# Optimization experiments

Hardware: AMD Instinct MI355X
Metric: run time of the kernel (lower is better)

Reference implementation:

```python
import jax, jax.numpy as jnp
import numpy as np

N_NODES = 100000
N_EDGES = 3200000
NEG_SLOPE = 0.2


def setup_inputs() -> dict:
    key = jax.random.key(0)
    k = jax.random.split(key, 7)
    feat = jax.random.normal(k[0], (N_NODES, 256), dtype=jnp.float32)
    W_fc = jax.random.normal(k[1], (64, 256), dtype=jnp.float32) * 0.05
    attn_l = jax.random.normal(k[2], (4, 16), dtype=jnp.float32) * 0.1
    attn_r = jax.random.normal(k[3], (4, 16), dtype=jnp.float32) * 0.1
    W_res = jax.random.normal(k[4], (64, 256), dtype=jnp.float32) * 0.05
    src = jax.random.randint(k[5], (N_EDGES,), 0, N_NODES, dtype=jnp.int32)
    dst = jax.random.randint(k[6], (N_EDGES,), 0, N_NODES, dtype=jnp.int32)
    return {"feat": feat, "W_fc": W_fc, "attn_l": attn_l, "attn_r": attn_r,
            "W_res": W_res, "src": src, "dst": dst}


def reference(feat, W_fc, attn_l, attn_r, W_res, src, dst):
    N = feat.shape[0]
    H, D = attn_l.shape
    # Linear projection -> per-head features [N, H, D]
    feat_src = (feat @ W_fc.T).reshape(N, H, D)
    # Per-node attention logits [N, H]
    el = jnp.einsum('nhd,hd->nh', feat_src, attn_l)
    er = jnp.einsum('nhd,hd->nh', feat_src, attn_r)
    # fused_gat: per-edge leaky-relu score, edge softmax over dst, scatter-sum
    e = jax.nn.leaky_relu(el[src] + er[dst], negative_slope=NEG_SLOPE)  # [E, H]
    emax = jax.ops.segment_max(e, dst, num_segments=N)  # [N, H]
    emax = jnp.where(jnp.isfinite(emax), emax, 0.0)  # zero-degree safety
    ee = jnp.exp(e - emax[dst])  # [E, H]
    denom = jax.ops.segment_sum(ee, dst, num_segments=N)  # [N, H]
    alpha = ee / jnp.maximum(denom[dst], 1e-20)  # [E, H]
    # weighted aggregation of source features -> [N, H, D]
    rst = jax.ops.segment_sum(alpha[:, :, None] * feat_src[src], dst,
                              num_segments=N)
    # residual connection (res_fc always present in this module)
    resval = (feat @ W_res.T).reshape(N, H, D)
    return rst + resval
```

## Files before the change

### kernel.cpp

```cpp
#include <hip/hip_runtime.h>
#include <hip/hip_bf16.h>


#define F_IN 256
#define O_OUT 64
#define NEG_SLOPE 0.2f
#define CHUNK 4096
#define RMAX 2048

using frag_ab = __attribute__((ext_vector_type(8))) short;
using frag_cd = __attribute__((ext_vector_type(4))) float;

__device__ __forceinline__ float lrelu(float x) {
    return x >= 0.0f ? x : NEG_SLOPE * x;
}

__device__ __forceinline__ unsigned short f2bf(float f) {
    unsigned int u = __float_as_uint(f);
    unsigned int r = (u + 0x7fffu + ((u >> 16) & 1u)) >> 16;
    return (unsigned short)r;
}
__device__ __forceinline__ float bflo(unsigned int p) {
    return __uint_as_float(p << 16);
}
__device__ __forceinline__ float bfhi(unsigned int p) {
    return __uint_as_float(p & 0xffff0000u);
}

__global__ __launch_bounds__(256) void wprep_kernel(
    const float* __restrict__ Wfc, const float* __restrict__ Wres,
    unsigned short* __restrict__ Bf)
{
    int tid = blockIdx.x * 256 + threadIdx.x;
    int ct = tid >> 9;
    int lane = tid & 63;
    int ks = (tid >> 6) & 7;
    int col = ct * 16 + (lane & 15);
    int kbase = ks * 32 + (lane >> 4) * 8;
    const float* srcW = (col < 64) ? (Wfc + (size_t)col * 256 + kbase)
                                   : (Wres + (size_t)(col - 64) * 256 + kbase);
    unsigned short* dstp = Bf + (size_t)tid * 8;
#pragma unroll
    for (int i = 0; i < 8; ++i) dstp[i] = f2bf(srcW[i]);
}

__global__ __launch_bounds__(256) void proj_mfma_kernel(
    const float* __restrict__ feat, const unsigned short* __restrict__ Bf,
    const float* __restrict__ attn_l, const float* __restrict__ attn_r,
    unsigned short* __restrict__ fsb, float* __restrict__ el,
    float* __restrict__ er, float* __restrict__ out,
    float* __restrict__ denom_zero, int N)
{
    __shared__ __align__(16) unsigned short sA[64 * 280];
    const int t = threadIdx.x;
    const int lane = t & 63;
    const int w = t >> 6;
    const int n0 = blockIdx.x * 64;
    if (n0 >= N) return;

    frag_ab bfrag[2][8];
    {
        const unsigned short* bp = Bf + (size_t)lane * 8;
#pragma unroll
        for (int j = 0; j < 2; ++j)
#pragma unroll
            for (int ks = 0; ks < 8; ++ks)
                bfrag[j][ks] = *(const frag_ab*)(bp + (size_t)((2 * w + j) * 8 + ks) * 512);
    }

    if (denom_zero && n0 * 4 + t < N * 4) denom_zero[n0 * 4 + t] = 0.0f;

    for (int i = 0; i < 8; ++i) {
        int f = i * 256 + t;
        int row = f >> 5, c8 = f & 31;
        int n = n0 + row;
        float4 v0 = make_float4(0.f, 0.f, 0.f, 0.f), v1 = v0;
        if (n < N) {
            const float4* p = (const float4*)(feat + (size_t)n * F_IN + c8 * 8);
            v0 = p[0]; v1 = p[1];
        }
        frag_ab pack;
        pack[0] = (short)f2bf(v0.x); pack[1] = (short)f2bf(v0.y);
        pack[2] = (short)f2bf(v0.z); pack[3] = (short)f2bf(v0.w);
        pack[4] = (short)f2bf(v1.x); pack[5] = (short)f2bf(v1.y);
        pack[6] = (short)f2bf(v1.z); pack[7] = (short)f2bf(v1.w);
        *(frag_ab*)(&sA[row * 280 + c8 * 8]) = pack;
    }
    __syncthreads();

    frag_cd acc[4][2];
#pragma unroll
    for (int rt = 0; rt < 4; ++rt)
#pragma unroll
        for (int j = 0; j < 2; ++j)
            acc[rt][j] = (frag_cd){0.f, 0.f, 0.f, 0.f};

#pragma unroll
    for (int ks = 0; ks < 8; ++ks) {
        frag_ab af[4];
#pragma unroll
        for (int rt = 0; rt < 4; ++rt) {
            int row = rt * 16 + (lane & 15);
            int c8 = ks * 4 + (lane >> 4);
            af[rt] = *(const frag_ab*)(&sA[row * 280 + c8 * 8]);
        }
#pragma unroll
        for (int rt = 0; rt < 4; ++rt)
#pragma unroll
            for (int j = 0; j < 2; ++j)
                acc[rt][j] = __builtin_amdgcn_mfma_f32_16x16x32_bf16(
                    af[rt], bfrag[j][ks], acc[rt][j], 0, 0, 0);
    }

    const int colq = lane & 15;
    const int quad = lane >> 4;
    if (w < 2) {
#pragma unroll
        for (int j = 0; j < 2; ++j) {
            int h = 2 * w + j;
            float al = attn_l[h * 16 + colq];
            float ar = attn_r[h * 16 + colq];
#pragma unroll
            for (int rt = 0; rt < 4; ++rt)
#pragma unroll
                for (int r = 0; r < 4; ++r) {
                    int node = n0 + rt * 16 + quad * 4 + r;
                    float v = acc[rt][j][r];
                    if (node < N) fsb[(size_t)node * O_OUT + h * 16 + colq] = f2bf(v);
                    float pl = v * al, pr = v * ar;
                    pl += __shfl_xor(pl, 1); pr += __shfl_xor(pr, 1);
                    pl += __shfl_xor(pl, 2); pr += __shfl_xor(pr, 2);
                    pl += __shfl_xor(pl, 4); pr += __shfl_xor(pr, 4);
                    pl += __shfl_xor(pl, 8); pr += __shfl_xor(pr, 8);
                    if (colq == 0 && node < N) {
                        el[(size_t)node * 4 + h] = pl;
                        er[(size_t)node * 4 + h] = pr;
                    }
                }
        }
    } else {
#pragma unroll
        for (int j = 0; j < 2; ++j) {
            int cb = 32 * (w - 2) + 16 * j;
#pragma unroll
            for (int rt = 0; rt < 4; ++rt)
#pragma unroll
                for (int r = 0; r < 4; ++r) {
                    int node = n0 + rt * 16 + quad * 4 + r;
                    if (node < N)
                        out[(size_t)node * O_OUT + cb + colq] = acc[rt][j][r];
                }
        }
    }
}

__global__ __launch_bounds__(256) void bucket_count_kernel(
    const int* __restrict__ dst, int* __restrict__ histT, int E, int B, int R)
{
    __shared__ int h[RMAX];
    int b = blockIdx.x, t = threadIdx.x;
    for (int i = t; i < R; i += 256) h[i] = 0;
    __syncthreads();
    int base = b * CHUNK;
    for (int i = t; i < CHUNK; i += 256) {
        int e = base + i;
        if (e < E) atomicAdd(&h[dst[e] >> 7], 1);
    }
    __syncthreads();
    for (int i = t; i < R; i += 256) histT[(size_t)i * B + b] = h[i];
}

__global__ __launch_bounds__(256) void scan_block_kernel(
    const int* __restrict__ counts, int* __restrict__ outp,
    int* __restrict__ bsums, int n)
{
    int t = threadIdx.x;
    int base = blockIdx.x * 1024 + t * 4;
    int c0 = 0, c1 = 0, c2 = 0, c3 = 0;
    if (base + 3 < n) {
        int4 v = *(const int4*)(counts + base);
        c0 = v.x; c1 = v.y; c2 = v.z; c3 = v.w;
    } else {
        if (base     < n) c0 = counts[base];
        if (base + 1 < n) c1 = counts[base + 1];
        if (base + 2 < n) c2 = counts[base + 2];
        if (base + 3 < n) c3 = counts[base + 3];
    }
    int tsum = c0 + c1 + c2 + c3;
    int inc = tsum;
    int lane = t & 63, wid = t >> 6;
#pragma unroll
    for (int o = 1; o < 64; o <<= 1) {
        int v = __shfl_up(inc, o);
        if (lane >= o) inc += v;
    }
    __shared__ int wsum[4];
    if (lane == 63) wsum[wid] = inc;
    __syncthreads();
    int woff = 0;
#pragma unroll
    for (int w = 0; w < 4; ++w)
        if (w < wid) woff += wsum[w];
    int excl = woff + inc - tsum;
    int e0 = excl, e1 = excl + c0, e2 = e1 + c1, e3 = e2 + c2;
    if (base + 3 < n) {
        *(int4*)(outp + base) = make_int4(e0, e1, e2, e3);
    } else {
        if (base     < n) outp[base]     = e0;
        if (base + 1 < n) outp[base + 1] = e1;
        if (base + 2 < n) outp[base + 2] = e2;
        if (base + 3 < n) outp[base + 3] = e3;
    }
    if (t == 255) bsums[blockIdx.x] = wsum[0] + wsum[1] + wsum[2] + wsum[3];
}

__global__ void scan_bsums_kernel(int* __restrict__ bsums, int nb)
{
    int lane = threadIdx.x;
    int carry = 0;
    for (int c = 0; c * 64 < nb; ++c) {
        int i = c * 64 + lane;
        int v = (i < nb) ? bsums[i] : 0;
        int inc = v;
#pragma unroll
        for (int o = 1; o < 64; o <<= 1) {
            int u = __shfl_up(inc, o);
            if (lane >= o) inc += u;
        }
        if (i < nb) bsums[i] = carry + inc - v;
        carry += __shfl(inc, 63);
    }
}

__global__ __launch_bounds__(256) void scan_final_kernel(
    int* __restrict__ outp, const int* __restrict__ bsums, int n, int total)
{
    int i = blockIdx.x * 256 + threadIdx.x;
    if (i < n) outp[i] = outp[i] + bsums[i >> 10];
    if (i == 0) outp[n] = total;
}

__global__ __launch_bounds__(256) void bucket_scatter_kernel(
    const int* __restrict__ src, const int* __restrict__ dst,
    const int* __restrict__ histS, unsigned int* __restrict__ sorted_pk,
    int E, int B, int R)
{
    __shared__ int h[RMAX];
    __shared__ int basebin[RMAX];
    int b = blockIdx.x, t = threadIdx.x;
    for (int i = t; i < R; i += 256) {
        h[i] = 0;
        basebin[i] = histS[(size_t)i * B + b];
    }
    __syncthreads();
    int base = b * CHUNK;
    for (int i = t; i < CHUNK; i += 256) {
        int e = base + i;
        if (e < E) {
            int d = dst[e];
            int bin = d >> 7;
            int rk = atomicAdd(&h[bin], 1);
            sorted_pk[basebin[bin] + rk] =
                ((unsigned int)src[e] << 7) | (unsigned int)(d & 127);
        }
    }
}

__global__ __launch_bounds__(512) void agg_bucket_kernel(
    const int* __restrict__ histS, const unsigned int* __restrict__ sorted_pk,
    const unsigned short* __restrict__ fsb, const float* __restrict__ el,
    const float* __restrict__ er, float* __restrict__ out,
    int N, int E, int B, int R)
{
    __shared__ int buf2[8192];
    __shared__ int hist[128], scn[128], cur[128];
    const int r = blockIdx.x;
    const int t = threadIdx.x;
    int start = histS[(size_t)r * B];
    int end = (r + 1 < R) ? histS[(size_t)(r + 1) * B] : E;
    if (start < 0) start = 0;
    if (end < start) end = start;
    if (end > E) end = E;
    const int cnt = end - start;

    if (t < 128) { hist[t] = 0; cur[t] = 0; }
    __syncthreads();
    for (int i = t; i < cnt; i += 512)
        atomicAdd(&hist[sorted_pk[start + i] & 127], 1);
    __syncthreads();
    if (t < 128) scn[t] = hist[t];
    __syncthreads();
    for (int o = 1; o < 128; o <<= 1) {
        int v = 0;
        if (t < 128 && t >= o) v = scn[t - o];
        __syncthreads();
        if (t < 128) scn[t] += v;
        __syncthreads();
    }
    const bool use_lds = (cnt <= 8192);
    if (use_lds) {
        for (int i = t; i < cnt; i += 512) {
            unsigned int pk = sorted_pk[start + i];
            int low = (int)(pk & 127u);
            int rk = atomicAdd(&cur[low], 1);
            buf2[(scn[low] - hist[low]) + rk] = (int)(pk >> 7);
        }
    }
    __syncthreads();

    const int lane = t & 63;
    const int w = t >> 6;
    const int half = lane >> 5;
    const int c = lane & 31;
    const int h = c >> 3;
    for (int j = 0; j < 16; ++j) {
        int dl = w * 16 + j;
        int d = r * 128 + dl;
        if (d >= N) break;
        const int k0 = scn[dl] - hist[dl];
        const int k1 = scn[dl];
        const float erh = er[(size_t)d * 4 + h];
        float a0 = 0.f, a1 = 0.f, den = 0.f;
        if (use_lds) {
            int kb = k0;
            for (; kb + 8 <= k1; kb += 8) {
                int s0 = buf2[kb + half];
                int s1 = buf2[kb + 2 + half];
                int s2 = buf2[kb + 4 + half];
                int s3 = buf2[kb + 6 + half];
                float e0 = el[(size_t)s0 * 4 + h];
                float e1 = el[(size_t)s1 * 4 + h];
                float e2 = el[(size_t)s2 * 4 + h];
                float e3 = el[(size_t)s3 * 4 + h];
                unsigned int f0 = *(const unsigned int*)(fsb + (size_t)s0 * O_OUT + 2 * c);
                unsigned int f1 = *(const unsigned int*)(fsb + (size_t)s1 * O_OUT + 2 * c);
                unsigned int f2 = *(const unsigned int*)(fsb + (size_t)s2 * O_OUT + 2 * c);
                unsigned int f3 = *(const unsigned int*)(fsb + (size_t)s3 * O_OUT + 2 * c);
                float w0 = __expf(lrelu(e0 + erh));
                float w1 = __expf(lrelu(e1 + erh));
                float w2 = __expf(lrelu(e2 + erh));
                float w3 = __expf(lrelu(e3 + erh));
                a0 += w0 * bflo(f0); a1 += w0 * bfhi(f0); den += w0;
                a0 += w1 * bflo(f1); a1 += w1 * bfhi(f1); den += w1;
                a0 += w2 * bflo(f2); a1 += w2 * bfhi(f2); den += w2;
                a0 += w3 * bflo(f3); a1 += w3 * bfhi(f3); den += w3;
            }
            for (; kb < k1; kb += 2) {
                int ki = kb + half;
                if (ki < k1) {
                    int s = buf2[ki];
                    float wv = __expf(lrelu(el[(size_t)s * 4 + h] + erh));
                    unsigned int f = *(const unsigned int*)(fsb + (size_t)s * O_OUT + 2 * c);
                    a0 += wv * bflo(f); a1 += wv * bfhi(f); den += wv;
                }
            }
        } else {
            for (int i2 = 0; i2 < cnt; i2 += 2) {
                int ki = i2 + half;
                if (ki < cnt) {
                    unsigned int pk = sorted_pk[start + ki];
                    if ((int)(pk & 127u) == dl) {
                        int s = (int)(pk >> 7);
                        float wv = __expf(lrelu(el[(size_t)s * 4 + h] + erh));
                        unsigned int f = *(const unsigned int*)(fsb + (size_t)s * O_OUT + 2 * c);
                        a0 += wv * bflo(f); a1 += wv * bfhi(f); den += wv;
                    }
                }
            }
        }
        a0 += __shfl_xor(a0, 32);
        a1 += __shfl_xor(a1, 32);
        den += __shfl_xor(den, 32);
        if (half == 0) {
            float inv = 1.0f / fmaxf(den, 1e-20f);
            float2* po = (float2*)(out + (size_t)d * O_OUT + 2 * c);
            float2 o = *po;
            o.x += a0 * inv;
            o.y += a1 * inv;
            *po = o;
        }
    }
}

__global__ __launch_bounds__(256) void edge_sum_kernel(
    const int* __restrict__ src, const int* __restrict__ dst,
    const float* __restrict__ el, const float* __restrict__ er,
    float* __restrict__ denom, int E)
{
    int e = blockIdx.x * 256 + threadIdx.x;
    if (e >= E) return;
    int s = src[e], d = dst[e];
    float4 l4 = ((const float4*)el)[s];
    float4 r4 = ((const float4*)er)[d];
    unsafeAtomicAdd(&denom[(size_t)d * 4 + 0], __expf(lrelu(l4.x + r4.x)));
    unsafeAtomicAdd(&denom[(size_t)d * 4 + 1], __expf(lrelu(l4.y + r4.y)));
    unsafeAtomicAdd(&denom[(size_t)d * 4 + 2], __expf(lrelu(l4.z + r4.z)));
    unsafeAtomicAdd(&denom[(size_t)d * 4 + 3], __expf(lrelu(l4.w + r4.w)));
}

__global__ __launch_bounds__(256) void agg_atomic_kernel(
    const int* __restrict__ src, const int* __restrict__ dst,
    const unsigned short* __restrict__ fsb, const float* __restrict__ el,
    const float* __restrict__ er, const float* __restrict__ denom,
    float* __restrict__ out, int E)
{
    const int lane = threadIdx.x & 63;
    const int wid = threadIdx.x >> 6;
    int e = blockIdx.x * 4 + wid;
    if (e >= E) return;
    int s = src[e], d = dst[e];
    int h = lane >> 4;
    float v = __expf(lrelu(el[(size_t)s * 4 + h] + er[(size_t)d * 4 + h]));
    float alpha = v / fmaxf(denom[(size_t)d * 4 + h], 1e-20f);
    float fval = __uint_as_float(((unsigned int)fsb[(size_t)s * O_OUT + lane]) << 16);
    unsafeAtomicAdd(&out[(size_t)d * O_OUT + lane], alpha * fval);
}

extern "C" void kernel_launch(void* const* d_in, const int* in_sizes, int n_in,
                              void* d_out, int out_size, void* d_ws, size_t ws_size,
                              hipStream_t stream) {
    const float* feat   = (const float*)d_in[0];
    const float* Wfc    = (const float*)d_in[1];
    const float* attn_l = (const float*)d_in[2];
    const float* attn_r = (const float*)d_in[3];
    const float* Wres   = (const float*)d_in[4];
    const int*   src    = (const int*)d_in[5];
    const int*   dst    = (const int*)d_in[6];

    const int N = in_sizes[0] / F_IN;
    const int E = in_sizes[5];
    float* out = (float*)d_out;

    const int R = (N + 127) >> 7;
    const int B = (E + CHUNK - 1) / CHUNK;
    const int nRB = R * B;
    const int nsb = (nRB + 1023) / 1024;

    float* el     = (float*)d_ws;
    float* er     = el + (size_t)N * 4;
    unsigned short* Bf = (unsigned short*)(er + (size_t)N * 4);
    int*   histT  = (int*)(Bf + 32768);
    int*   histS  = histT + nRB;
    int*   bsums  = histS + nRB + 8;
    unsigned int* sorted_pk = (unsigned int*)(bsums + 1024);
    unsigned short* fsb = (unsigned short*)(sorted_pk + E);
    size_t need_main = (size_t)((char*)(fsb + (size_t)N * O_OUT) - (char*)d_ws);

    int nproj = (N + 63) / 64;

    if (ws_size >= need_main && R <= RMAX && nsb <= 1024) {
        wprep_kernel<<<16, 256, 0, stream>>>(Wfc, Wres, Bf);
        proj_mfma_kernel<<<nproj, 256, 0, stream>>>(
            feat, Bf, attn_l, attn_r, fsb, el, er, out, nullptr, N);
        bucket_count_kernel<<<B, 256, 0, stream>>>(dst, histT, E, B, R);
        scan_block_kernel<<<nsb, 256, 0, stream>>>(histT, histS, bsums, nRB);
        scan_bsums_kernel<<<1, 64, 0, stream>>>(bsums, nsb);
        scan_final_kernel<<<(nRB + 255) / 256, 256, 0, stream>>>(histS, bsums, nRB, E);
        bucket_scatter_kernel<<<B, 256, 0, stream>>>(src, dst, histS, sorted_pk, E, B, R);
        agg_bucket_kernel<<<R, 512, 0, stream>>>(
            histS, sorted_pk, fsb, el, er, out, N, E, B, R);
    } else {
        float* denom = (float*)histT;
        unsigned short* fsb2 = (unsigned short*)(denom + (size_t)N * 4);
        wprep_kernel<<<16, 256, 0, stream>>>(Wfc, Wres, Bf);
        proj_mfma_kernel<<<nproj, 256, 0, stream>>>(
            feat, Bf, attn_l, attn_r, fsb2, el, er, out, denom, N);
        edge_sum_kernel<<<(E + 255) / 256, 256, 0, stream>>>(src, dst, el, er, denom, E);
        agg_atomic_kernel<<<(E + 3) / 4, 256, 0, stream>>>(
            src, dst, fsb2, el, er, denom, out, E);
    }
}
```

Before: 428.8 us.

## Shrink destination buckets to 64 nodes and deepen gather unroll to 16

Destination buckets shrink from 128 to 64 nodes, giving twice as many aggregation blocks of 256 threads each, with half the LDS per block. This is meant to improve occupancy and load balance in the gather-heavy aggregation kernel. The inner edge loop also gains a 16-edge unrolled stage so more independent feature loads are in flight. In exchange the bucket histogram doubles in size (R*B entries), which adds scan work and memory traffic, and the bsums buffer and its limit are enlarged to match.

```diff
diff --git a/kernel.cpp b/kernel.cpp
--- a/kernel.cpp
+++ b/kernel.cpp
@@ -7,6 +7,8 @@
 #define NEG_SLOPE 0.2f
 #define CHUNK 4096
 #define RMAX 2048
+#define BSH 6
+#define BSZ 64
 
 using frag_ab = __attribute__((ext_vector_type(8))) short;
 using frag_cd = __attribute__((ext_vector_type(4))) float;
@@ -164,7 +166,7 @@
     int base = b * CHUNK;
     for (int i = t; i < CHUNK; i += 256) {
         int e = base + i;
-        if (e < E) atomicAdd(&h[dst[e] >> 7], 1);
+        if (e < E) atomicAdd(&h[dst[e] >> BSH], 1);
     }
     __syncthreads();
     for (int i = t; i < R; i += 256) histT[(size_t)i * B + b] = h[i];
@@ -258,22 +260,22 @@
         int e = base + i;
         if (e < E) {
             int d = dst[e];
-            int bin = d >> 7;
+            int bin = d >> BSH;
             int rk = atomicAdd(&h[bin], 1);
             sorted_pk[basebin[bin] + rk] =
-                ((unsigned int)src[e] << 7) | (unsigned int)(d & 127);
-        }
-    }
-}
-
-__global__ __launch_bounds__(512) void agg_bucket_kernel(
+                ((unsigned int)src[e] << BSH) | (unsigned int)(d & (BSZ - 1));
+        }
+    }
+}
+
+__global__ __launch_bounds__(256) void agg_bucket_kernel(
     const int* __restrict__ histS, const unsigned int* __restrict__ sorted_pk,
     const unsigned short* __restrict__ fsb, const float* __restrict__ el,
     const float* __restrict__ er, float* __restrict__ out,
     int N, int E, int B, int R)
 {
-    __shared__ int buf2[8192];
-    __shared__ int hist[128], scn[128], cur[128];
+    __shared__ int buf2[4096];
+    __shared__ int hist[BSZ], scn[BSZ], cur[BSZ];
     const int r = blockIdx.x;
     const int t = threadIdx.x;
     int start = histS[(size_t)r * B];
@@ -283,27 +285,27 @@
     if (end > E) end = E;
     const int cnt = end - start;
 
-    if (t < 128) { hist[t] = 0; cur[t] = 0; }
-    __syncthreads();
-    for (int i = t; i < cnt; i += 512)
-        atomicAdd(&hist[sorted_pk[start + i] & 127], 1);
-    __syncthreads();
-    if (t < 128) scn[t] = hist[t];
-    __syncthreads();
-    for (int o = 1; o < 128; o <<= 1) {
+    if (t < BSZ) { hist[t] = 0; cur[t] = 0; }
+    __syncthreads();
+    for (int i = t; i < cnt; i += 256)
+        atomicAdd(&hist[sorted_pk[start + i] & (BSZ - 1)], 1);
+    __syncthreads();
+    if (t < BSZ) scn[t] = hist[t];
+    __syncthreads();
+    for (int o = 1; o < BSZ; o <<= 1) {
         int v = 0;
-        if (t < 128 && t >= o) v = scn[t - o];
+        if (t < BSZ && t >= o) v = scn[t - o];
         __syncthreads();
-        if (t < 128) scn[t] += v;
+        if (t < BSZ) scn[t] += v;
         __syncthreads();
     }
-    const bool use_lds = (cnt <= 8192);
+    const bool use_lds = (cnt <= 4096);
     if (use_lds) {
-        for (int i = t; i < cnt; i += 512) {
+        for (int i = t; i < cnt; i += 256) {
             unsigned int pk = sorted_pk[start + i];
-            int low = (int)(pk & 127u);
+            int low = (int)(pk & (BSZ - 1));
             int rk = atomicAdd(&cur[low], 1);
-            buf2[(scn[low] - hist[low]) + rk] = (int)(pk >> 7);
+            buf2[(scn[low] - hist[low]) + rk] = (int)(pk >> BSH);
         }
     }
     __syncthreads();
@@ -315,7 +317,7 @@
     const int h = c >> 3;
     for (int j = 0; j < 16; ++j) {
         int dl = w * 16 + j;
-        int d = r * 128 + dl;
+        int d = r * BSZ + dl;
         if (d >= N) break;
         const int k0 = scn[dl] - hist[dl];
         const int k1 = scn[dl];
@@ -323,6 +325,48 @@
         float a0 = 0.f, a1 = 0.f, den = 0.f;
         if (use_lds) {
             int kb = k0;
+            for (; kb + 16 <= k1; kb += 16) {
+                int s0 = buf2[kb + 0 + half];
+                int s1 = buf2[kb + 2 + half];
+                int s2 = buf2[kb + 4 + half];
+                int s3 = buf2[kb + 6 + half];
+                int s4 = buf2[kb + 8 + half];
+                int s5 = buf2[kb + 10 + half];
+                int s6 = buf2[kb + 12 + half];
+                int s7 = buf2[kb + 14 + half];
+                float e0 = el[(size_t)s0 * 4 + h];
+                float e1 = el[(size_t)s1 * 4 + h];
+                float e2 = el[(size_t)s2 * 4 + h];
+                float e3 = el[(size_t)s3 * 4 + h];
+                float e4 = el[(size_t)s4 * 4 + h];
+                float e5 = el[(size_t)s5 * 4 + h];
+                float e6 = el[(size_t)s6 * 4 + h];
+                float e7 = el[(size_t)s7 * 4 + h];
+                unsigned int f0 = *(const unsigned int*)(fsb + (size_t)s0 * O_OUT + 2 * c);
+                unsigned int f1 = *(const unsigned int*)(fsb + (size_t)s1 * O_OUT + 2 * c);
+                unsigned int f2 = *(const unsigned int*)(fsb + (size_t)s2 * O_OUT + 2 * c);
+                unsigned int f3 = *(const unsigned int*)(fsb + (size_t)s3 * O_OUT + 2 * c);
+                unsigned int f4 = *(const unsigned int*)(fsb + (size_t)s4 * O_OUT + 2 * c);
+                unsigned int f5 = *(const unsigned int*)(fsb + (size_t)s5 * O_OUT + 2 * c);
+                unsigned int f6 = *(const unsigned int*)(fsb + (size_t)s6 * O_OUT + 2 * c);
+                unsigned int f7 = *(const unsigned int*)(fsb + (size_t)s7 * O_OUT + 2 * c);
+                float w0 = __expf(lrelu(e0 + erh));
+                float w1 = __expf(lrelu(e1 + erh));
+                float w2 = __expf(lrelu(e2 + erh));
+                float w3 = __expf(lrelu(e3 + erh));
+                float w4 = __expf(lrelu(e4 + erh));
+                float w5 = __expf(lrelu(e5 + erh));
+                float w6 = __expf(lrelu(e6 + erh));
+                float w7 = __expf(lrelu(e7 + erh));
+                a0 += w0 * bflo(f0); a1 += w0 * bfhi(f0); den += w0;
+                a0 += w1 * bflo(f1); a1 += w1 * bfhi(f1); den += w1;
+                a0 += w2 * bflo(f2); a1 += w2 * bfhi(f2); den += w2;
+                a0 += w3 * bflo(f3); a1 += w3 * bfhi(f3); den += w3;
+                a0 += w4 * bflo(f4); a1 += w4 * bfhi(f4); den += w4;
+                a0 += w5 * bflo(f5); a1 += w5 * bfhi(f5); den += w5;
+                a0 += w6 * bflo(f6); a1 += w6 * bfhi(f6); den += w6;
+                a0 += w7 * bflo(f7); a1 += w7 * bfhi(f7); den += w7;
+            }
             for (; kb + 8 <= k1; kb += 8) {
                 int s0 = buf2[kb + half];
                 int s1 = buf2[kb + 2 + half];
@@ -359,8 +403,8 @@
                 int ki = i2 + half;
                 if (ki < cnt) {
                     unsigned int pk = sorted_pk[start + ki];
-                    if ((int)(pk & 127u) == dl) {
-                        int s = (int)(pk >> 7);
+                    if ((int)(pk & (BSZ - 1)) == dl) {
+                        int s = (int)(pk >> BSH);
                         float wv = __expf(lrelu(el[(size_t)s * 4 + h] + erh));
                         unsigned int f = *(const unsigned int*)(fsb + (size_t)s * O_OUT + 2 * c);
                         a0 += wv * bflo(f); a1 += wv * bfhi(f); den += wv;
@@ -431,7 +475,7 @@
     const int E = in_sizes[5];
     float* out = (float*)d_out;
 
-    const int R = (N + 127) >> 7;
+    const int R = (N + BSZ - 1) >> BSH;
     const int B = (E + CHUNK - 1) / CHUNK;
     const int nRB = R * B;
     const int nsb = (nRB + 1023) / 1024;
@@ -442,13 +486,13 @@
     int*   histT  = (int*)(Bf + 32768);
     int*   histS  = histT + nRB;
     int*   bsums  = histS + nRB + 8;
-    unsigned int* sorted_pk = (unsigned int*)(bsums + 1024);
+    unsigned int* sorted_pk = (unsigned int*)(bsums + 2048);
     unsigned short* fsb = (unsigned short*)(sorted_pk + E);
     size_t need_main = (size_t)((char*)(fsb + (size_t)N * O_OUT) - (char*)d_ws);
 
     int nproj = (N + 63) / 64;
 
-    if (ws_size >= need_main && R <= RMAX && nsb <= 1024) {
+    if (ws_size >= need_main && R <= RMAX && nsb <= 2048) {
         wprep_kernel<<<16, 256, 0, stream>>>(Wfc, Wres, Bf);
         proj_mfma_kernel<<<nproj, 256, 0, stream>>>(
             feat, Bf, attn_l, attn_r, fsb, el, er, out, nullptr, N);
@@ -457,7 +501,7 @@
         scan_bsums_kernel<<<1, 64, 0, stream>>>(bsums, nsb);
         scan_final_kernel<<<(nRB + 255) / 256, 256, 0, stream>>>(histS, bsums, nRB, E);
         bucket_scatter_kernel<<<B, 256, 0, stream>>>(src, dst, histS, sorted_pk, E, B, R);
-        agg_bucket_kernel<<<R, 512, 0, stream>>>(
+        agg_bucket_kernel<<<R, 256, 0, stream>>>(
             histS, sorted_pk, fsb, el, er, out, N, E, B, R);
     } else {
         float* denom = (float*)histT;
```

Result: slower. 439.1 us (+2.4%).
